# Kernel optimization log

Hardware: AMD Instinct MI355X
Metric: run time of the kernel (lower is better)

The kernel has to match this reference:

```python
import jax, jax.numpy as jnp
import numpy as np

B, S, D, H = 2, 2048, 64, 12  # batch, seq, richness (per-head dim), heads
NEG = -99999.0


def setup_inputs() -> dict:
    key = jax.random.key(0)
    ks = jax.random.split(key, 9)
    s_in = 1.0 / np.sqrt(D)
    s_out = 1.0 / np.sqrt(H * D)
    return {
        "x": jax.random.normal(ks[0], (B, S, D), dtype=jnp.float32),
        "Wq": jax.random.uniform(ks[1], (D, H * D), jnp.float32, -s_in, s_in),
        "bq": jax.random.uniform(ks[2], (H * D,), jnp.float32, -s_in, s_in),
        "Wk": jax.random.uniform(ks[3], (D, H * D), jnp.float32, -s_in, s_in),
        "bk": jax.random.uniform(ks[4], (H * D,), jnp.float32, -s_in, s_in),
        "Wv": jax.random.uniform(ks[5], (D, H * D), jnp.float32, -s_in, s_in),
        "bv": jax.random.uniform(ks[6], (H * D,), jnp.float32, -s_in, s_in),
        "Wo": jax.random.uniform(ks[7], (H * D, D), jnp.float32, -s_out, s_out),
        "bo": jax.random.uniform(ks[8], (D,), jnp.float32, -s_out, s_out),
    }


def reference(x, Wq, bq, Wk, bk, Wv, bv, Wo, bo):
    b, s, d = x.shape
    def split_heads(y):
        return y.reshape(b, s, H, d).transpose(0, 2, 1, 3)  # [B,H,S,D]
    q = split_heads(x @ Wq + bq)
    k = split_heads(x @ Wk + bk)
    v = split_heads(x @ Wv + bv)
    # NOTE: no 1/sqrt(d) scaling, faithful to original module.
    scores = jnp.einsum("bhqd,bhkd->bhqk", q, k)  # [B,H,S,S]
    # Faithful quirky mask: tril of the scores, then mask where it's zero.
    mask = jnp.tril(scores)
    scores = jnp.where(mask == 0, NEG, scores)
    p = jax.nn.softmax(scores, axis=-1)
    o = jnp.einsum("bhqk,bhkd->bhqd", p, v)  # [B,H,S,D]
    o = o.transpose(0, 2, 1, 3).reshape(b, s, H * d)
    return o @ Wo + bo
```

## Files before the change

kernel.cpp:

```cpp
#include <hip/hip_runtime.h>
#include <math.h>
#include <type_traits>

#define BB 2
#define SS 2048
#define DD 64
#define HH 12
#define C2FIX 23.083120654223414f

typedef _Float16 v8h __attribute__((ext_vector_type(8)));
typedef short    v8s __attribute__((ext_vector_type(8)));
typedef float    v4f __attribute__((ext_vector_type(4)));
typedef unsigned int v2u __attribute__((ext_vector_type(2)));

__device__ __forceinline__ unsigned short f2bf(float f) {
    unsigned u = __float_as_uint(f);
    u += 0x7FFF + ((u >> 16) & 1);
    return (unsigned short)(u >> 16);
}

__device__ __forceinline__ void async16(const void* g, void* l) {
    __builtin_amdgcn_global_load_lds(
        (const __attribute__((address_space(1))) unsigned int*)g,
        (__attribute__((address_space(3))) unsigned int*)l, 16, 0, 0);
}

__global__ __launch_bounds__(256) void prep_kernel(
    const float* __restrict__ x,
    const float* __restrict__ Wq, const float* __restrict__ Wk,
    const float* __restrict__ Wv, const float* __restrict__ Wo,
    _Float16* __restrict__ x16, _Float16* __restrict__ W16,
    _Float16* __restrict__ WoT)
{
    const int idx = blockIdx.x * 256 + threadIdx.x;
    if (idx < 262144) {
        x16[idx] = (_Float16)x[idx];
    } else if (idx < 262144 + 147456) {
        const int t = idx - 262144;
        const int k = t / 2304, c = t % 2304;
        const int mat = c / 768, cc = c % 768;
        const float* W = (mat == 0) ? Wq : (mat == 1) ? Wk : Wv;
        W16[c * 64 + k] = (_Float16)W[k * 768 + cc];
    } else {
        const int e = idx - 262144 - 147456;
        WoT[(e & 63) * 768 + (e >> 6)] = (_Float16)Wo[e];
    }
}

__global__ __launch_bounds__(256) void qkv_kernel(
    const _Float16* __restrict__ x16, const _Float16* __restrict__ W16,
    const float* __restrict__ bq, const float* __restrict__ bk,
    const float* __restrict__ bv,
    _Float16* __restrict__ Q16, _Float16* __restrict__ K16,
    unsigned short* __restrict__ VT)
{
    const int r0  = blockIdx.x * 64;
    const int c0g = blockIdx.y * 64;
    const int mat = c0g / 768, cc0 = c0g % 768;
    const int h   = cc0 >> 6;
    const int b   = r0 >> 11, s0 = r0 & 2047;

    const int wave = threadIdx.x >> 6, lane = threadIdx.x & 63;
    const int llow = lane & 15, quad = lane >> 4;
    const int rowbase = r0 + 16 * wave;

    const float* bias = (mat == 0) ? bq : (mat == 1) ? bk : bv;

    v8h a0 = *(const v8h*)(x16 + (size_t)(rowbase + llow) * 64 + quad * 8);
    v8h a1 = *(const v8h*)(x16 + (size_t)(rowbase + llow) * 64 + 32 + quad * 8);

    v4f acc[4];
    float bv4[4];
#pragma unroll
    for (int nb = 0; nb < 4; nb++) {
        const int col = c0g + 16 * nb + llow;
        v8h b0 = *(const v8h*)(W16 + (size_t)col * 64 + quad * 8);
        v8h b1 = *(const v8h*)(W16 + (size_t)col * 64 + 32 + quad * 8);
        v4f a = (v4f){0.f, 0.f, 0.f, 0.f};
        a = __builtin_amdgcn_mfma_f32_16x16x32_f16(a0, b0, a, 0, 0, 0);
        a = __builtin_amdgcn_mfma_f32_16x16x32_f16(a1, b1, a, 0, 0, 0);
        acc[nb] = a;
        bv4[nb] = bias[cc0 + 16 * nb + llow];
    }

    const int bh = b * HH + h;
    if (mat == 0) {
#pragma unroll
        for (int nb = 0; nb < 4; nb++)
#pragma unroll
            for (int r = 0; r < 4; r++) {
                const int s = s0 + 16 * wave + quad * 4 + r;
                Q16[((size_t)bh * SS + s) * 64 + 16 * nb + llow] =
                    (_Float16)((acc[nb][r] + bv4[nb]) * 1.4426950408889634f);
            }
    } else if (mat == 1) {
#pragma unroll
        for (int nb = 0; nb < 4; nb++)
#pragma unroll
            for (int r = 0; r < 4; r++) {
                const int s = s0 + 16 * wave + quad * 4 + r;
                K16[((size_t)bh * SS + s) * 64 + 16 * nb + llow] =
                    (_Float16)(acc[nb][r] + bv4[nb]);
            }
    } else {
#pragma unroll
        for (int nb = 0; nb < 4; nb++) {
            const int d = 16 * nb + llow;
            const int s = s0 + 16 * wave + quad * 4;
            unsigned short p0 = f2bf(acc[nb][0] + bv4[nb]);
            unsigned short p1 = f2bf(acc[nb][1] + bv4[nb]);
            unsigned short p2 = f2bf(acc[nb][2] + bv4[nb]);
            unsigned short p3 = f2bf(acc[nb][3] + bv4[nb]);
            v2u pk = (v2u){(unsigned)p0 | ((unsigned)p1 << 16),
                           (unsigned)p2 | ((unsigned)p3 << 16)};
            *(v2u*)&VT[((size_t)bh * 64 + d) * SS + s] = pk;
        }
    }
}

__global__ __launch_bounds__(256, 4) void attn_kernel(
    const _Float16* __restrict__ Q16, const _Float16* __restrict__ K16,
    const unsigned short* __restrict__ VTg, _Float16* __restrict__ O16)
{
    __shared__ __align__(16) _Float16       Kl[2][64 * 64];
    __shared__ __align__(16) unsigned short Vl[2][64 * 64];
    __shared__ __align__(16) unsigned short Pl[4][16 * 64];

    const int bh    = blockIdx.y;
    const int qtile = (int)((blockIdx.x + 11 * blockIdx.y) & 31);
    const int qBase = qtile * 64;
    const int wave  = threadIdx.x >> 6;
    const int lane  = threadIdx.x & 63;
    const int llow  = lane & 15;
    const int quad  = lane >> 4;
    const int q0    = qBase + 16 * wave;

    const _Float16*       Kp = K16 + (size_t)bh * SS * 64;
    const unsigned short* Vp = VTg + (size_t)bh * 64 * SS;

    const _Float16* Qp = Q16 + ((size_t)bh * SS + q0) * 64;
    v8h qa0 = *(const v8h*)(Qp + llow * 64 + quad * 8);
    v8h qa1 = *(const v8h*)(Qp + llow * 64 + 32 + quad * 8);

    v4f o[4];
    float lacc = 0.f;
#pragma unroll
    for (int nb = 0; nb < 4; nb++) o[nb] = (v4f){0.f, 0.f, 0.f, 0.f};

    const int nt = qtile + 1;
    const int qrow = q0 + llow;
    const int sw = llow & 7;

#pragma unroll
    for (int rep = 0; rep < 2; rep++) {
        int c = rep * 256 + threadIdx.x;
        int row = c >> 3, g = (c & 7) ^ (row & 7);
        async16(Kp + (size_t)row * 64 + g * 8, &Kl[0][(rep * 256 + wave * 64) * 8]);
        async16(Vp + (size_t)row * SS + g * 8, &Vl[0][(rep * 256 + wave * 64) * 8]);
    }

    auto tile_body = [&](int t, auto masked_c) {
        constexpr bool MASKED = decltype(masked_c)::value;
        __syncthreads();
        if (t + 1 < nt) {
            const int ktn = (t + 1) * 64, bufn = (t + 1) & 1;
#pragma unroll
            for (int rep = 0; rep < 2; rep++) {
                int c = rep * 256 + threadIdx.x;
                int row = c >> 3, g = (c & 7) ^ (row & 7);
                async16(Kp + (size_t)(ktn + row) * 64 + g * 8,
                        &Kl[bufn][(rep * 256 + wave * 64) * 8]);
                async16(Vp + (size_t)row * SS + ktn + g * 8,
                        &Vl[bufn][(rep * 256 + wave * 64) * 8]);
            }
        }
        const int buf = t & 1, kt = t * 64;

        v4f sc[4];
#pragma unroll
        for (int cb = 0; cb < 4; cb++) {
            const int rk = 16 * cb + llow;
            v8h k0 = *(const v8h*)&Kl[buf][rk * 64 + ((quad ^ sw)) * 8];
            v8h k1 = *(const v8h*)&Kl[buf][rk * 64 + (((4 + quad) ^ sw)) * 8];
            v4f a = (v4f){0.f, 0.f, 0.f, 0.f};
            a = __builtin_amdgcn_mfma_f32_16x16x32_f16(k0, qa0, a, 0, 0, 0);
            a = __builtin_amdgcn_mfma_f32_16x16x32_f16(k1, qa1, a, 0, 0, 0);
            sc[cb] = a;
        }

#pragma unroll
        for (int cb = 0; cb < 4; cb++) {
            const int kbase = kt + 16 * cb + quad * 4;
            unsigned dw[2];
#pragma unroll
            for (int h2 = 0; h2 < 2; h2++) {
                unsigned lo = 0, hi = 0;
#pragma unroll
                for (int j2 = 0; j2 < 2; j2++) {
                    const int r = h2 * 2 + j2;
                    const float sv = sc[cb][r];
                    const float e  = __builtin_amdgcn_exp2f(sv - C2FIX);
                    float p;
                    if constexpr (MASKED)
                        p = (kbase + r <= qrow && sv != 0.f) ? e : 0.f;
                    else
                        p = (sv != 0.f) ? e : 0.f;
                    lacc += p;
                    if (j2 == 0) lo = __float_as_uint(p);
                    else         hi = __float_as_uint(p);
                }
                dw[h2] = (lo >> 16) | (hi & 0xFFFF0000u);
            }
            *(v2u*)&Pl[wave][llow * 64 + (((2 * cb + (quad >> 1)) ^ sw) * 8)
                             + (quad & 1) * 4] = (v2u){dw[0], dw[1]};
        }

        v8s pa0 = *(const v8s*)&Pl[wave][llow * 64 + ((quad ^ sw) * 8)];
        v8s pa1 = *(const v8s*)&Pl[wave][llow * 64 + (((4 + quad) ^ sw) * 8)];

#pragma unroll
        for (int nb = 0; nb < 4; nb++) {
            const int rv = 16 * nb + llow;
            v8s vv0 = *(const v8s*)&Vl[buf][rv * 64 + ((quad ^ sw)) * 8];
            v8s vv1 = *(const v8s*)&Vl[buf][rv * 64 + (((4 + quad) ^ sw)) * 8];
            o[nb] = __builtin_amdgcn_mfma_f32_16x16x32_bf16(pa0, vv0, o[nb], 0, 0, 0);
            o[nb] = __builtin_amdgcn_mfma_f32_16x16x32_bf16(pa1, vv1, o[nb], 0, 0, 0);
        }
    };

    for (int t = 0; t < nt - 1; t++) tile_body(t, std::false_type{});
    tile_body(nt - 1, std::true_type{});

    lacc += __shfl_xor(lacc, 16);
    lacc += __shfl_xor(lacc, 32);
    float lr[4];
#pragma unroll
    for (int r = 0; r < 4; r++)
        lr[r] = __shfl(lacc, quad * 4 + r);
    _Float16* Op = O16 + ((size_t)bh * SS + q0) * 64;
#pragma unroll
    for (int nb = 0; nb < 4; nb++)
#pragma unroll
        for (int r = 0; r < 4; r++)
            Op[(quad * 4 + r) * 64 + 16 * nb + llow] = (_Float16)(o[nb][r] / lr[r]);
}

__global__ __launch_bounds__(256) void out_kernel(
    const _Float16* __restrict__ O16, const _Float16* __restrict__ WoT,
    const float* __restrict__ bo, float* __restrict__ out)
{
    __shared__ __align__(16) float red[4][16][66];
    const int r0   = blockIdx.x * 16;
    const int wave = threadIdx.x >> 6, lane = threadIdx.x & 63;
    const int llow = lane & 15, quad = lane >> 4;
    const int b = r0 >> 11, s = r0 & 2047;

    v4f acc[4];
#pragma unroll
    for (int cb = 0; cb < 4; cb++) acc[cb] = (v4f){0.f, 0.f, 0.f, 0.f};

#pragma unroll
    for (int i = 0; i < 6; i++) {
        const int kb = wave * 6 + i;
        const int h = kb >> 1, dseg = (kb & 1) * 32;
        v8h af = *(const v8h*)(O16 + ((size_t)(b * HH + h) * SS + s + llow) * 64 + dseg + quad * 8);
#pragma unroll
        for (int cb = 0; cb < 4; cb++) {
            v8h bf = *(const v8h*)(WoT + (size_t)(16 * cb + llow) * 768 + kb * 32 + quad * 8);
            acc[cb] = __builtin_amdgcn_mfma_f32_16x16x32_f16(af, bf, acc[cb], 0, 0, 0);
        }
    }

#pragma unroll
    for (int cb = 0; cb < 4; cb++)
#pragma unroll
        for (int r = 0; r < 4; r++)
            red[wave][quad * 4 + r][16 * cb + llow] = acc[cb][r];
    __syncthreads();

    const int col = threadIdx.x & 63, rr = threadIdx.x >> 6;
    const float bias = bo[col];
    for (int i = rr; i < 16; i += 4) {
        float sum = red[0][i][col] + red[1][i][col] + red[2][i][col] + red[3][i][col] + bias;
        out[(size_t)(r0 + i) * 64 + col] = sum;
    }
}

extern "C" void kernel_launch(void* const* d_in, const int* in_sizes, int n_in,
                              void* d_out, int out_size, void* d_ws, size_t ws_size,
                              hipStream_t stream)
{
    const float* x  = (const float*)d_in[0];
    const float* Wq = (const float*)d_in[1];
    const float* bq = (const float*)d_in[2];
    const float* Wk = (const float*)d_in[3];
    const float* bk = (const float*)d_in[4];
    const float* Wv = (const float*)d_in[5];
    const float* bv = (const float*)d_in[6];
    const float* Wo = (const float*)d_in[7];
    const float* bo = (const float*)d_in[8];
    float* out = (float*)d_out;

    char* w = (char*)d_ws;
    const size_t MB = 1024 * 1024;
    _Float16*       x16 = (_Float16*)(w);
    _Float16*       W16 = (_Float16*)(w + 512 * 1024);
    _Float16*       WoT = (_Float16*)(w + 832 * 1024);
    _Float16*       Q16 = (_Float16*)(w + 1 * MB);
    _Float16*       K16 = (_Float16*)(w + 7 * MB);
    unsigned short* VT  = (unsigned short*)(w + 13 * MB);
    _Float16*       O16 = (_Float16*)(w + 19 * MB);

    prep_kernel<<<1792, 256, 0, stream>>>(x, Wq, Wk, Wv, Wo, x16, W16, WoT);
    qkv_kernel<<<dim3(64, 36), 256, 0, stream>>>(x16, W16, bq, bk, bv, Q16, K16, VT);
    attn_kernel<<<dim3(32, BB * HH), 256, 0, stream>>>(Q16, K16, VT, O16);
    out_kernel<<<(BB * SS) / 16, 256, 0, stream>>>(O16, WoT, bo, out);
}
```

Baseline: 133.0 us.

## Fuse x conversion into QKV, vectorize Q/K stores, remap attention grid per XCD

Drops the separate fp32-to-fp16 conversion of x in the prep kernel and converts x inline in the QKV kernel, removing one pass over x. For Q and K the MFMA operands are swapped so each lane holds four consecutive columns, which allows packed 4-wide fp16 stores and vector bias loads instead of scattered scalar stores. The attention grid is flattened to 1D and remapped so each XCD handles three heads, with q-tiles ordered to balance causal work across them. The per-element division in the output normalisation becomes a multiply by a reciprocal.

```diff
diff --git a/kernel.cpp b/kernel.cpp
--- a/kernel.cpp
+++ b/kernel.cpp
@@ -9,6 +9,7 @@
 #define C2FIX 23.083120654223414f
 
 typedef _Float16 v8h __attribute__((ext_vector_type(8)));
+typedef _Float16 v4h __attribute__((ext_vector_type(4)));
 typedef short    v8s __attribute__((ext_vector_type(8)));
 typedef float    v4f __attribute__((ext_vector_type(4)));
 typedef unsigned int v2u __attribute__((ext_vector_type(2)));
@@ -26,29 +27,24 @@
 }
 
 __global__ __launch_bounds__(256) void prep_kernel(
-    const float* __restrict__ x,
     const float* __restrict__ Wq, const float* __restrict__ Wk,
     const float* __restrict__ Wv, const float* __restrict__ Wo,
-    _Float16* __restrict__ x16, _Float16* __restrict__ W16,
-    _Float16* __restrict__ WoT)
+    _Float16* __restrict__ W16, _Float16* __restrict__ WoT)
 {
     const int idx = blockIdx.x * 256 + threadIdx.x;
-    if (idx < 262144) {
-        x16[idx] = (_Float16)x[idx];
-    } else if (idx < 262144 + 147456) {
-        const int t = idx - 262144;
-        const int k = t / 2304, c = t % 2304;
+    if (idx < 147456) {
+        const int k = idx / 2304, c = idx % 2304;
         const int mat = c / 768, cc = c % 768;
         const float* W = (mat == 0) ? Wq : (mat == 1) ? Wk : Wv;
         W16[c * 64 + k] = (_Float16)W[k * 768 + cc];
     } else {
-        const int e = idx - 262144 - 147456;
+        const int e = idx - 147456;
         WoT[(e & 63) * 768 + (e >> 6)] = (_Float16)Wo[e];
     }
 }
 
 __global__ __launch_bounds__(256) void qkv_kernel(
-    const _Float16* __restrict__ x16, const _Float16* __restrict__ W16,
+    const float* __restrict__ x, const _Float16* __restrict__ W16,
     const float* __restrict__ bq, const float* __restrict__ bk,
     const float* __restrict__ bv,
     _Float16* __restrict__ Q16, _Float16* __restrict__ K16,
@@ -64,53 +60,68 @@
     const int llow = lane & 15, quad = lane >> 4;
     const int rowbase = r0 + 16 * wave;
 
-    const float* bias = (mat == 0) ? bq : (mat == 1) ? bk : bv;
-
-    v8h a0 = *(const v8h*)(x16 + (size_t)(rowbase + llow) * 64 + quad * 8);
-    v8h a1 = *(const v8h*)(x16 + (size_t)(rowbase + llow) * 64 + 32 + quad * 8);
+    const float* xr = x + (size_t)(rowbase + llow) * 64 + quad * 8;
+    v4f x0 = *(const v4f*)xr,        x1 = *(const v4f*)(xr + 4);
+    v4f x2 = *(const v4f*)(xr + 32), x3 = *(const v4f*)(xr + 36);
+    v8h a0, a1;
+#pragma unroll
+    for (int j = 0; j < 4; j++) {
+        a0[j] = (_Float16)x0[j]; a0[4 + j] = (_Float16)x1[j];
+        a1[j] = (_Float16)x2[j]; a1[4 + j] = (_Float16)x3[j];
+    }
 
     v4f acc[4];
-    float bv4[4];
 #pragma unroll
     for (int nb = 0; nb < 4; nb++) {
         const int col = c0g + 16 * nb + llow;
         v8h b0 = *(const v8h*)(W16 + (size_t)col * 64 + quad * 8);
         v8h b1 = *(const v8h*)(W16 + (size_t)col * 64 + 32 + quad * 8);
         v4f a = (v4f){0.f, 0.f, 0.f, 0.f};
-        a = __builtin_amdgcn_mfma_f32_16x16x32_f16(a0, b0, a, 0, 0, 0);
-        a = __builtin_amdgcn_mfma_f32_16x16x32_f16(a1, b1, a, 0, 0, 0);
+        if (mat != 2) {
+            a = __builtin_amdgcn_mfma_f32_16x16x32_f16(b0, a0, a, 0, 0, 0);
+            a = __builtin_amdgcn_mfma_f32_16x16x32_f16(b1, a1, a, 0, 0, 0);
+        } else {
+            a = __builtin_amdgcn_mfma_f32_16x16x32_f16(a0, b0, a, 0, 0, 0);
+            a = __builtin_amdgcn_mfma_f32_16x16x32_f16(a1, b1, a, 0, 0, 0);
+        }
         acc[nb] = a;
-        bv4[nb] = bias[cc0 + 16 * nb + llow];
     }
 
     const int bh = b * HH + h;
     if (mat == 0) {
-#pragma unroll
-        for (int nb = 0; nb < 4; nb++)
-#pragma unroll
-            for (int r = 0; r < 4; r++) {
-                const int s = s0 + 16 * wave + quad * 4 + r;
-                Q16[((size_t)bh * SS + s) * 64 + 16 * nb + llow] =
-                    (_Float16)((acc[nb][r] + bv4[nb]) * 1.4426950408889634f);
-            }
+        const int srow = s0 + 16 * wave + llow;
+        _Float16* qp = Q16 + ((size_t)bh * SS + srow) * 64 + quad * 4;
+#pragma unroll
+        for (int nb = 0; nb < 4; nb++) {
+            const v4f bb = *(const v4f*)(bq + cc0 + 16 * nb + quad * 4);
+            v4h pk;
+#pragma unroll
+            for (int rr = 0; rr < 4; rr++)
+                pk[rr] = (_Float16)((acc[nb][rr] + bb[rr]) * 1.4426950408889634f);
+            *(v4h*)(qp + 16 * nb) = pk;
+        }
     } else if (mat == 1) {
-#pragma unroll
-        for (int nb = 0; nb < 4; nb++)
-#pragma unroll
-            for (int r = 0; r < 4; r++) {
-                const int s = s0 + 16 * wave + quad * 4 + r;
-                K16[((size_t)bh * SS + s) * 64 + 16 * nb + llow] =
-                    (_Float16)(acc[nb][r] + bv4[nb]);
-            }
+        const int srow = s0 + 16 * wave + llow;
+        _Float16* kp = K16 + ((size_t)bh * SS + srow) * 64 + quad * 4;
+#pragma unroll
+        for (int nb = 0; nb < 4; nb++) {
+            const v4f bb = *(const v4f*)(bk + cc0 + 16 * nb + quad * 4);
+            v4h pk;
+#pragma unroll
+            for (int rr = 0; rr < 4; rr++)
+                pk[rr] = (_Float16)(acc[nb][rr] + bb[rr]);
+            *(v4h*)(kp + 16 * nb) = pk;
+        }
     } else {
 #pragma unroll
         for (int nb = 0; nb < 4; nb++) {
+            const float bs = bv[cc0 + 16 * nb + llow];
             const int d = 16 * nb + llow;
             const int s = s0 + 16 * wave + quad * 4;
-            unsigned short p0 = f2bf(acc[nb][0] + bv4[nb]);
-            unsigned short p1 = f2bf(acc[nb][1] + bv4[nb]);
-            unsigned short p2 = f2bf(acc[nb][2] + bv4[nb]);
-            unsigned short p3 = f2bf(acc[nb][3] + bv4[nb]);
+            unsigned short p0 = f2bf(acc[nb][0] + bs);
+            unsigned short p1 = f2bf(acc[nb][1] + bs);
+            unsigned short p2 = f2bf(acc[nb][2] + bs);
+            unsigned short p3 = f2bf(acc[nb][3] + bs);
             v2u pk = (v2u){(unsigned)p0 | ((unsigned)p1 << 16),
                            (unsigned)p2 | ((unsigned)p3 << 16)};
             *(v2u*)&VT[((size_t)bh * 64 + d) * SS + s] = pk;
@@ -126,8 +137,16 @@
     __shared__ __align__(16) unsigned short Vl[2][64 * 64];
     __shared__ __align__(16) unsigned short Pl[4][16 * 64];
 
-    const int bh    = blockIdx.y;
-    const int qtile = (int)((blockIdx.x + 11 * blockIdx.y) & 31);
+    const int L   = blockIdx.x;
+    const int xcd = L & 7;
+    const int u   = L >> 3;
+    const int a   = u & 31;
+    const int tt  = u >> 5;
+    const int bh  = xcd * 3 + tt;
+    const int qtile = (tt == 0) ? a
+                    : (tt == 1) ? ((a + 16) & 31)
+                    : ((a < 16) ? (30 - 2 * a) : (63 - 2 * a));
+
     const int qBase = qtile * 64;
     const int wave  = threadIdx.x >> 6;
     const int lane  = threadIdx.x & 63;
@@ -182,10 +201,10 @@
             const int rk = 16 * cb + llow;
             v8h k0 = *(const v8h*)&Kl[buf][rk * 64 + ((quad ^ sw)) * 8];
             v8h k1 = *(const v8h*)&Kl[buf][rk * 64 + (((4 + quad) ^ sw)) * 8];
-            v4f a = (v4f){0.f, 0.f, 0.f, 0.f};
-            a = __builtin_amdgcn_mfma_f32_16x16x32_f16(k0, qa0, a, 0, 0, 0);
-            a = __builtin_amdgcn_mfma_f32_16x16x32_f16(k1, qa1, a, 0, 0, 0);
-            sc[cb] = a;
+            v4f a2 = (v4f){0.f, 0.f, 0.f, 0.f};
+            a2 = __builtin_amdgcn_mfma_f32_16x16x32_f16(k0, qa0, a2, 0, 0, 0);
+            a2 = __builtin_amdgcn_mfma_f32_16x16x32_f16(k1, qa1, a2, 0, 0, 0);
+            sc[cb] = a2;
         }
 
 #pragma unroll
@@ -237,12 +256,16 @@
 #pragma unroll
     for (int r = 0; r < 4; r++)
         lr[r] = __shfl(lacc, quad * 4 + r);
+    float ir[4];
+#pragma unroll
+    for (int r = 0; r < 4; r++)
+        ir[r] = 1.0f / lr[r];
     _Float16* Op = O16 + ((size_t)bh * SS + q0) * 64;
 #pragma unroll
     for (int nb = 0; nb < 4; nb++)
 #pragma unroll
         for (int r = 0; r < 4; r++)
-            Op[(quad * 4 + r) * 64 + 16 * nb + llow] = (_Float16)(o[nb][r] / lr[r]);
+            Op[(quad * 4 + r) * 64 + 16 * nb + llow] = (_Float16)(o[nb][r] * ir[r]);
 }
 
 __global__ __launch_bounds__(256) void out_kernel(
@@ -303,7 +326,6 @@
 
     char* w = (char*)d_ws;
     const size_t MB = 1024 * 1024;
-    _Float16*       x16 = (_Float16*)(w);
     _Float16*       W16 = (_Float16*)(w + 512 * 1024);
     _Float16*       WoT = (_Float16*)(w + 832 * 1024);
     _Float16*       Q16 = (_Float16*)(w + 1 * MB);
@@ -311,8 +333,8 @@
     unsigned short* VT  = (unsigned short*)(w + 13 * MB);
     _Float16*       O16 = (_Float16*)(w + 19 * MB);
 
-    prep_kernel<<<1792, 256, 0, stream>>>(x, Wq, Wk, Wv, Wo, x16, W16, WoT);
-    qkv_kernel<<<dim3(64, 36), 256, 0, stream>>>(x16, W16, bq, bk, bv, Q16, K16, VT);
-    attn_kernel<<<dim3(32, BB * HH), 256, 0, stream>>>(Q16, K16, VT, O16);
+    prep_kernel<<<768, 256, 0, stream>>>(Wq, Wk, Wv, Wo, W16, WoT);
+    qkv_kernel<<<dim3(64, 36), 256, 0, stream>>>(x, W16, bq, bk, bv, Q16, K16, VT);
+    attn_kernel<<<768, 256, 0, stream>>>(Q16, K16, VT, O16);
     out_kernel<<<(BB * SS) / 16, 256, 0, stream>>>(O16, WoT, bo, out);
 }
```

New measurement: 141.3 us. +6.2%, slower.
